# Kernel optimization log

Hardware: AMD Instinct MI355X
Metric: run time of the kernel (lower is better)

The kernel has to match this reference:

```python
import jax, jax.numpy as jnp
import numpy as np
import math

D_K = 64
DROP_P = 0.5

def setup_inputs() -> dict:
    key = jax.random.key(0)
    kq, kk, kv, km = jax.random.split(key, 4)
    B, S, d = 32, 2048, D_K
    Q = jax.random.normal(kq, (B, S, d), dtype=jnp.float32)
    K = jax.random.normal(kk, (B, S, d), dtype=jnp.float32)
    V = jax.random.normal(kv, (B, S, d), dtype=jnp.float32)
    # Bernoulli(keep_prob) mask for training-mode dropout (p=0.5)
    dropout_mask = jax.random.bernoulli(km, 1.0 - DROP_P, (B, S, S))
    return {"Q": Q, "K": K, "V": V, "dropout_mask": dropout_mask}

def reference(Q, K, V, dropout_mask):
    # attn = softmax(Q K^T / sqrt(d_k)); dropout; y = attn V
    scale = 1.0 / math.sqrt(D_K)
    scores = jnp.einsum('bqd,bkd->bqk', Q, K) * scale   # [B,S,S]
    attn = jax.nn.softmax(scores, axis=-1)
    keep_scale = 1.0 / (1.0 - DROP_P)
    attn = jnp.where(dropout_mask, attn * keep_scale, 0.0)
    y = jnp.einsum('bqk,bkd->bqd', attn, V)             # [B,S,d]
    return (y, attn)
```

## Files before the change

kernel.cpp:

```cpp
#include <hip/hip_runtime.h>
#include <hip/hip_bf16.h>
#include <stdint.h>

#define SQ 2048
#define DK 64
#define NB 32
#define TQ 16
#define EW 2064
#define NTHREADS 512
#define SCL 0.18033688011112042f

typedef __attribute__((ext_vector_type(8))) short short8;
typedef __attribute__((ext_vector_type(4))) float f32x4;

__device__ __forceinline__ unsigned f2bf_u(float x) {
    unsigned u = __builtin_bit_cast(unsigned, x);
    u += 0x7fffu + ((u >> 16) & 1u);
    return u >> 16;
}
__device__ __forceinline__ float bf2f(unsigned h) {
    return __builtin_bit_cast(float, h << 16);
}
__device__ __forceinline__ void split8(const float* p, short8& h, short8& l) {
    f32x4 a = *(const f32x4*)p;
    f32x4 b = *(const f32x4*)(p + 4);
    #pragma unroll
    for (int j = 0; j < 4; ++j) {
        unsigned ua = f2bf_u(a[j]);
        h[j] = (short)ua; l[j] = (short)f2bf_u(a[j] - bf2f(ua));
        unsigned ub = f2bf_u(b[j]);
        h[j + 4] = (short)ub; l[j + 4] = (short)f2bf_u(b[j] - bf2f(ub));
    }
}
__device__ __forceinline__ unsigned pkf16(float a, float b) {
    unsigned short ha = __builtin_bit_cast(unsigned short, (_Float16)a);
    unsigned short hb = __builtin_bit_cast(unsigned short, (_Float16)b);
    return (unsigned)ha | ((unsigned)hb << 16);
}
__device__ __forceinline__ float upk16(unsigned u, int hi) {
    return (float)__builtin_bit_cast(_Float16, (unsigned short)(hi ? (u >> 16) : (u & 0xffffu)));
}

__global__ __launch_bounds__(256) void prep_kernel(
    const float* __restrict__ K, const float* __restrict__ V,
    unsigned short* __restrict__ Khi, unsigned short* __restrict__ Klo,
    unsigned short* __restrict__ Vt)
{
    __shared__ float vtile[64][65];
    const int t  = threadIdx.x;
    const int b  = blockIdx.x >> 5;
    const int s0 = (blockIdx.x & 31) << 6;
    const size_t base = ((size_t)b * SQ + s0) * DK + (size_t)t * 16;

    {
        short8 h0, l0, h1, l1;
        split8(K + base,     h0, l0);
        split8(K + base + 8, h1, l1);
        *(short8*)(Khi + base)     = h0;
        *(short8*)(Khi + base + 8) = h1;
        *(short8*)(Klo + base)     = l0;
        *(short8*)(Klo + base + 8) = l1;
    }
    {
        const int sr = t >> 2, dc = (t & 3) << 4;
        #pragma unroll
        for (int u = 0; u < 16; u += 4) {
            f32x4 v = *(const f32x4*)(V + base + u);
            vtile[sr][dc + u + 0] = v[0];
            vtile[sr][dc + u + 1] = v[1];
            vtile[sr][dc + u + 2] = v[2];
            vtile[sr][dc + u + 3] = v[3];
        }
    }
    __syncthreads();
    #pragma unroll
    for (int rep = 0; rep < 16; ++rep) {
        const int idx = rep * 256 + t;
        const int d = idx >> 6, s = idx & 63;
        Vt[((size_t)b * DK + d) * SQ + s0 + s] = (unsigned short)f2bf_u(vtile[s][d]);
    }
}

__global__ __launch_bounds__(NTHREADS, 4) void sdpa_main(
    const float* __restrict__ Q, const unsigned short* __restrict__ Khi,
    const unsigned short* __restrict__ Klo, const unsigned short* __restrict__ Vt,
    const unsigned* __restrict__ Mk, float* __restrict__ Yout, float* __restrict__ Aout)
{
    __shared__ __align__(16) unsigned short e_lds[TQ][EW];
    __shared__ float yp[2][TQ][DK];
    __shared__ float rsum[8][TQ];
    __shared__ float i2s[TQ];

    const int tid  = threadIdx.x;
    const int lane = tid & 63;
    const int wv   = tid >> 6;
    const int m16  = lane & 15;
    const int kq   = lane >> 4;
    const int koff = kq * 8;

    const int b  = blockIdx.x >> 7;
    const int q0 = (blockIdx.x & 127) * TQ;

    short8 qh[2], ql[2];
    {
        const float* qrow = Q + ((size_t)b * SQ + q0 + m16) * DK;
        split8(qrow + koff,      qh[0], ql[0]);
        split8(qrow + 32 + koff, qh[1], ql[1]);
    }

    float rs = 0.f;
    {
        const size_t krow = ((size_t)b * SQ + wv * 256 + m16) * DK;
        const unsigned short* khp = Khi + krow;
        const unsigned short* klp = Klo + krow;
        for (int t = 0; t < 16; ++t) {
            const int off = t * 16 * DK;
            f32x4 acc = {0.f, 0.f, 0.f, 0.f};
            #pragma unroll
            for (int c = 0; c < 2; ++c) {
                short8 kh = *(const short8*)(khp + off + c * 32 + koff);
                short8 kl = *(const short8*)(klp + off + c * 32 + koff);
                acc = __builtin_amdgcn_mfma_f32_16x16x32_bf16(kh, qh[c], acc, 0, 0, 0);
                acc = __builtin_amdgcn_mfma_f32_16x16x32_bf16(kh, ql[c], acc, 0, 0, 0);
                acc = __builtin_amdgcn_mfma_f32_16x16x32_bf16(kl, qh[c], acc, 0, 0, 0);
            }
            const float e0 = exp2f(acc[0] * SCL);
            const float e1 = exp2f(acc[1] * SCL);
            const float e2 = exp2f(acc[2] * SCL);
            const float e3 = exp2f(acc[3] * SCL);
            rs += (e0 + e1) + (e2 + e3);
            uint2 pk;
            pk.x = pkf16(e0, e1);
            pk.y = pkf16(e2, e3);
            *(uint2*)&e_lds[m16][wv * 256 + t * 16 + kq * 4] = pk;
        }
    }
    rs += __shfl_xor(rs, 16);
    rs += __shfl_xor(rs, 32);
    if (lane < 16) rsum[wv][lane] = rs;
    __syncthreads();

    if (tid < 16) {
        float s = 0.f;
        #pragma unroll
        for (int w = 0; w < 8; ++w) s += rsum[w][tid];
        i2s[tid] = 2.0f / s;
    }
    __syncthreads();

    {
        const size_t g0 = ((size_t)b * SQ + q0) * SQ + (size_t)tid * 4;
        #pragma unroll 2
        for (int r = 0; r < TQ; ++r) {
            const uint4 mk = *(const uint4*)(Mk + g0 + (size_t)r * SQ);
            const uint2 ev = *(const uint2*)&e_lds[r][tid * 4];
            const float i2 = i2s[r];
            const float a0 = mk.x ? upk16(ev.x, 0) * i2 : 0.f;
            const float a1 = mk.y ? upk16(ev.x, 1) * i2 : 0.f;
            const float a2 = mk.z ? upk16(ev.y, 0) * i2 : 0.f;
            const float a3 = mk.w ? upk16(ev.y, 1) * i2 : 0.f;
            f32x4 av = {a0, a1, a2, a3};
            *(f32x4*)(Aout + g0 + (size_t)r * SQ) = av;
            uint2 pb;
            pb.x = f2bf_u(a0) | (f2bf_u(a1) << 16);
            pb.y = f2bf_u(a2) | (f2bf_u(a3) << 16);
            *(uint2*)&e_lds[r][tid * 4] = pb;
        }
    }
    __syncthreads();

    {
        const int khalf = wv & 1;
        const int d0 = (wv >> 1) * 16;
        const unsigned short* vrow = Vt + ((size_t)b * DK + d0 + m16) * SQ;
        f32x4 acc = {0.f, 0.f, 0.f, 0.f};
        for (int ch = 0; ch < 32; ++ch) {
            const int k0 = khalf * 1024 + ch * 32;
            short8 af = *(const short8*)&e_lds[m16][k0 + koff];
            short8 vf = *(const short8*)(vrow + k0 + koff);
            acc = __builtin_amdgcn_mfma_f32_16x16x32_bf16(af, vf, acc, 0, 0, 0);
        }
        #pragma unroll
        for (int r = 0; r < 4; ++r)
            yp[khalf][kq * 4 + r][d0 + m16] = acc[r];
    }
    __syncthreads();

    {
        const int q  = tid >> 5;
        const int dd = (tid & 31) * 2;
        float2 yv;
        yv.x = yp[0][q][dd]     + yp[1][q][dd];
        yv.y = yp[0][q][dd + 1] + yp[1][q][dd + 1];
        *(float2*)(Yout + ((size_t)b * SQ + q0 + q) * DK + dd) = yv;
    }
}

extern "C" void kernel_launch(void* const* d_in, const int* in_sizes, int n_in,
                              void* d_out, int out_size, void* d_ws, size_t ws_size,
                              hipStream_t stream) {
    const float*    Q  = (const float*)d_in[0];
    const float*    K  = (const float*)d_in[1];
    const float*    V  = (const float*)d_in[2];
    const unsigned* Mk = (const unsigned*)d_in[3];
    float* Yout = (float*)d_out;
    float* Aout = (float*)d_out + (size_t)NB * SQ * DK;

    const size_t NEL = (size_t)NB * SQ * DK;
    unsigned short* Khi = (unsigned short*)d_ws;
    unsigned short* Klo = Khi + NEL;
    unsigned short* Vt  = Klo + NEL;

    prep_kernel<<<dim3(NB * (SQ / 64)), dim3(256), 0, stream>>>(K, V, Khi, Klo, Vt);
    sdpa_main<<<dim3(NB * (SQ / TQ)), dim3(NTHREADS), 0, stream>>>(
        Q, Khi, Klo, Vt, Mk, Yout, Aout);
}
```

Before: 507.6 us.

## Pipeline mask/attn-finish with PV MFMA per chunk, swizzle LDS, nontemporal IO

The dropout/normalize pass that writes the attention matrix is split into eight 256-column chunks, and each chunk is software-pipelined with the PV MFMA accumulation of the previous chunk. This lets mask loads and attention stores overlap tensor work instead of running as a separate phase. LDS addresses are XOR-swizzled to cut bank conflicts, and mask loads and output stores use nontemporal hints. The Y reduction is also restructured so each wave pair sums its partials. The cost is more barriers (one per chunk) and changed per-thread work mapping.

```diff
diff --git a/kernel.cpp b/kernel.cpp
--- a/kernel.cpp
+++ b/kernel.cpp
@@ -12,6 +12,8 @@
 
 typedef __attribute__((ext_vector_type(8))) short short8;
 typedef __attribute__((ext_vector_type(4))) float f32x4;
+typedef __attribute__((ext_vector_type(4))) unsigned u32x4;
+typedef __attribute__((ext_vector_type(2))) unsigned u32x2;
 
 __device__ __forceinline__ unsigned f2bf_u(float x) {
     unsigned u = __builtin_bit_cast(unsigned, x);
@@ -87,7 +89,7 @@
     const unsigned* __restrict__ Mk, float* __restrict__ Yout, float* __restrict__ Aout)
 {
     __shared__ __align__(16) unsigned short e_lds[TQ][EW];
-    __shared__ float yp[2][TQ][DK];
+    __shared__ float yp[4][TQ][16];
     __shared__ float rsum[8][TQ];
     __shared__ float i2s[TQ];
 
@@ -113,6 +115,7 @@
         const size_t krow = ((size_t)b * SQ + wv * 256 + m16) * DK;
         const unsigned short* khp = Khi + krow;
         const unsigned short* klp = Klo + krow;
+        const int xw = (m16 & 7) << 3;
         for (int t = 0; t < 16; ++t) {
             const int off = t * 16 * DK;
             f32x4 acc = {0.f, 0.f, 0.f, 0.f};
@@ -129,17 +132,16 @@
             const float e2 = exp2f(acc[2] * SCL);
             const float e3 = exp2f(acc[3] * SCL);
             rs += (e0 + e1) + (e2 + e3);
-            uint2 pk;
-            pk.x = pkf16(e0, e1);
-            pk.y = pkf16(e2, e3);
-            *(uint2*)&e_lds[m16][wv * 256 + t * 16 + kq * 4] = pk;
+            u32x2 pk;
+            pk[0] = pkf16(e0, e1);
+            pk[1] = pkf16(e2, e3);
+            *(u32x2*)&e_lds[m16][(wv * 256 + t * 16 + kq * 4) ^ xw] = pk;
         }
     }
     rs += __shfl_xor(rs, 16);
     rs += __shfl_xor(rs, 32);
     if (lane < 16) rsum[wv][lane] = rs;
     __syncthreads();
-
     if (tid < 16) {
         float s = 0.f;
         #pragma unroll
@@ -148,52 +150,80 @@
     }
     __syncthreads();
 
-    {
-        const size_t g0 = ((size_t)b * SQ + q0) * SQ + (size_t)tid * 4;
-        #pragma unroll 2
-        for (int r = 0; r < TQ; ++r) {
-            const uint4 mk = *(const uint4*)(Mk + g0 + (size_t)r * SQ);
-            const uint2 ev = *(const uint2*)&e_lds[r][tid * 4];
-            const float i2 = i2s[r];
-            const float a0 = mk.x ? upk16(ev.x, 0) * i2 : 0.f;
-            const float a1 = mk.y ? upk16(ev.x, 1) * i2 : 0.f;
-            const float a2 = mk.z ? upk16(ev.y, 0) * i2 : 0.f;
-            const float a3 = mk.w ? upk16(ev.y, 1) * i2 : 0.f;
-            f32x4 av = {a0, a1, a2, a3};
-            *(f32x4*)(Aout + g0 + (size_t)r * SQ) = av;
-            uint2 pb;
-            pb.x = f2bf_u(a0) | (f2bf_u(a1) << 16);
-            pb.y = f2bf_u(a2) | (f2bf_u(a3) << 16);
-            *(uint2*)&e_lds[r][tid * 4] = pb;
-        }
-    }
-    __syncthreads();
-
-    {
-        const int khalf = wv & 1;
-        const int d0 = (wv >> 1) * 16;
-        const unsigned short* vrow = Vt + ((size_t)b * DK + d0 + m16) * SQ;
-        f32x4 acc = {0.f, 0.f, 0.f, 0.f};
-        for (int ch = 0; ch < 32; ++ch) {
-            const int k0 = khalf * 1024 + ch * 32;
-            short8 af = *(const short8*)&e_lds[m16][k0 + koff];
+    const int cr = tid >> 5;
+    const int cc = (tid & 31) * 8;
+    const int xc = (cr & 7) << 3;
+    const float i2 = i2s[cr];
+    const size_t crow = ((size_t)b * SQ + q0 + cr) * SQ + cc;
+
+    const int g   = wv >> 1;
+    const int par = wv & 1;
+    const int xm  = (m16 & 7) << 3;
+    const unsigned short* vrow = Vt + ((size_t)b * DK + g * 16 + m16) * SQ;
+    f32x4 acc = {0.f, 0.f, 0.f, 0.f};
+
+    #define C_FINISH(s, ma, mb)                                                   \
+    {                                                                             \
+        unsigned short* ep = &e_lds[cr][((s) * 256 + cc) ^ xc];                   \
+        const u32x4 ev = *(const u32x4*)ep;                                       \
+        const float a0 = (ma)[0] ? upk16(ev[0], 0) * i2 : 0.f;                    \
+        const float a1 = (ma)[1] ? upk16(ev[0], 1) * i2 : 0.f;                    \
+        const float a2 = (ma)[2] ? upk16(ev[1], 0) * i2 : 0.f;                    \
+        const float a3 = (ma)[3] ? upk16(ev[1], 1) * i2 : 0.f;                    \
+        const float a4 = (mb)[0] ? upk16(ev[2], 0) * i2 : 0.f;                    \
+        const float a5 = (mb)[1] ? upk16(ev[2], 1) * i2 : 0.f;                    \
+        const float a6 = (mb)[2] ? upk16(ev[3], 0) * i2 : 0.f;                    \
+        const float a7 = (mb)[3] ? upk16(ev[3], 1) * i2 : 0.f;                    \
+        f32x4 av0 = {a0, a1, a2, a3};                                             \
+        f32x4 av1 = {a4, a5, a6, a7};                                             \
+        __builtin_nontemporal_store(av0, (f32x4*)(Aout + crow + (s) * 256));      \
+        __builtin_nontemporal_store(av1, (f32x4*)(Aout + crow + (s) * 256 + 4));  \
+        u32x4 pb;                                                                 \
+        pb[0] = f2bf_u(a0) | (f2bf_u(a1) << 16);                                  \
+        pb[1] = f2bf_u(a2) | (f2bf_u(a3) << 16);                                  \
+        pb[2] = f2bf_u(a4) | (f2bf_u(a5) << 16);                                  \
+        pb[3] = f2bf_u(a6) | (f2bf_u(a7) << 16);                                  \
+        *(u32x4*)ep = pb;                                                         \
+    }
+
+    {
+        u32x4 ma = __builtin_nontemporal_load((const u32x4*)(Mk + crow));
+        u32x4 mb = __builtin_nontemporal_load((const u32x4*)(Mk + crow + 4));
+        C_FINISH(0, ma, mb);
+    }
+    __syncthreads();
+
+    for (int s = 0; s < 8; ++s) {
+        u32x4 na, nb;
+        if (s < 7) {
+            na = __builtin_nontemporal_load((const u32x4*)(Mk + crow + (s + 1) * 256));
+            nb = __builtin_nontemporal_load((const u32x4*)(Mk + crow + (s + 1) * 256 + 4));
+        }
+        #pragma unroll
+        for (int c = 0; c < 4; ++c) {
+            const int k0 = s * 256 + par * 128 + c * 32;
+            short8 af = *(const short8*)&e_lds[m16][(k0 + koff) ^ xm];
             short8 vf = *(const short8*)(vrow + k0 + koff);
             acc = __builtin_amdgcn_mfma_f32_16x16x32_bf16(af, vf, acc, 0, 0, 0);
         }
-        #pragma unroll
-        for (int r = 0; r < 4; ++r)
-            yp[khalf][kq * 4 + r][d0 + m16] = acc[r];
-    }
-    __syncthreads();
-
-    {
-        const int q  = tid >> 5;
-        const int dd = (tid & 31) * 2;
-        float2 yv;
-        yv.x = yp[0][q][dd]     + yp[1][q][dd];
-        yv.y = yp[0][q][dd + 1] + yp[1][q][dd + 1];
-        *(float2*)(Yout + ((size_t)b * SQ + q0 + q) * DK + dd) = yv;
-    }
+        if (s < 7) C_FINISH(s + 1, na, nb);
+        __syncthreads();
+    }
+
+    if (par == 1) {
+        #pragma unroll
+        for (int r = 0; r < 4; ++r) yp[g][kq * 4 + r][m16] = acc[r];
+    }
+    __syncthreads();
+    if (par == 0) {
+        #pragma unroll
+        for (int r = 0; r < 4; ++r) {
+            const float yv = acc[r] + yp[g][kq * 4 + r][m16];
+            __builtin_nontemporal_store(yv,
+                Yout + ((size_t)b * SQ + q0 + kq * 4 + r) * DK + g * 16 + m16);
+        }
+    }
+    #undef C_FINISH
 }
 
 extern "C" void kernel_launch(void* const* d_in, const int* in_sizes, int n_in,
```

Result: no change. 498.6 us (-1.8%).

## Split fused attention into QK/softmax kernel and separate PV kernel rereading attn

Applied to the files above, without the earlier changes.

Splits the fused kernel in two. The first kernel computes the scores, writes exp values as bf16 into LDS with an XOR swizzle, and emits the dropout-masked attention matrix using nontemporal loads and stores. The second kernel rereads the fp32 attention matrix from global memory, converts it to bf16 and does the PV MFMA to produce Y. Both kernels remap block indices so that each XCD handles whole batches, and the QK MFMA chain is split into two accumulators. The aim is to cut LDS pressure and dependency stalls, at the cost of reading the 512MB attention matrix back from global memory a second time.

```diff
diff --git a/kernel.cpp b/kernel.cpp
--- a/kernel.cpp
+++ b/kernel.cpp
@@ -7,11 +7,12 @@
 #define NB 32
 #define TQ 16
 #define EW 2064
-#define NTHREADS 512
 #define SCL 0.18033688011112042f
 
 typedef __attribute__((ext_vector_type(8))) short short8;
 typedef __attribute__((ext_vector_type(4))) float f32x4;
+typedef __attribute__((ext_vector_type(4))) unsigned u32x4;
+typedef __attribute__((ext_vector_type(2))) unsigned u32x2;
 
 __device__ __forceinline__ unsigned f2bf_u(float x) {
     unsigned u = __builtin_bit_cast(unsigned, x);
@@ -20,6 +21,9 @@
 }
 __device__ __forceinline__ float bf2f(unsigned h) {
     return __builtin_bit_cast(float, h << 16);
+}
+__device__ __forceinline__ float bf2f_hi(unsigned u) {
+    return __builtin_bit_cast(float, u & 0xffff0000u);
 }
 __device__ __forceinline__ void split8(const float* p, short8& h, short8& l) {
     f32x4 a = *(const f32x4*)p;
@@ -31,14 +35,6 @@
         unsigned ub = f2bf_u(b[j]);
         h[j + 4] = (short)ub; l[j + 4] = (short)f2bf_u(b[j] - bf2f(ub));
     }
-}
-__device__ __forceinline__ unsigned pkf16(float a, float b) {
-    unsigned short ha = __builtin_bit_cast(unsigned short, (_Float16)a);
-    unsigned short hb = __builtin_bit_cast(unsigned short, (_Float16)b);
-    return (unsigned)ha | ((unsigned)hb << 16);
-}
-__device__ __forceinline__ float upk16(unsigned u, int hi) {
-    return (float)__builtin_bit_cast(_Float16, (unsigned short)(hi ? (u >> 16) : (u & 0xffffu)));
 }
 
 __global__ __launch_bounds__(256) void prep_kernel(
@@ -81,13 +77,12 @@
     }
 }
 
-__global__ __launch_bounds__(NTHREADS, 4) void sdpa_main(
+__global__ __launch_bounds__(512, 4) void qk_kernel(
     const float* __restrict__ Q, const unsigned short* __restrict__ Khi,
-    const unsigned short* __restrict__ Klo, const unsigned short* __restrict__ Vt,
-    const unsigned* __restrict__ Mk, float* __restrict__ Yout, float* __restrict__ Aout)
+    const unsigned short* __restrict__ Klo, const unsigned* __restrict__ Mk,
+    float* __restrict__ Aout)
 {
     __shared__ __align__(16) unsigned short e_lds[TQ][EW];
-    __shared__ float yp[2][TQ][DK];
     __shared__ float rsum[8][TQ];
     __shared__ float i2s[TQ];
 
@@ -98,8 +93,11 @@
     const int kq   = lane >> 4;
     const int koff = kq * 8;
 
-    const int b  = blockIdx.x >> 7;
-    const int q0 = (blockIdx.x & 127) * TQ;
+    const int bx  = blockIdx.x;
+    const int xcd = bx & 7;
+    const int j   = bx >> 3;
+    const int b   = xcd * 4 + (j >> 7);
+    const int q0  = (j & 127) * TQ;
 
     short8 qh[2], ql[2];
     {
@@ -113,33 +111,36 @@
         const size_t krow = ((size_t)b * SQ + wv * 256 + m16) * DK;
         const unsigned short* khp = Khi + krow;
         const unsigned short* klp = Klo + krow;
+        const int xw = (m16 & 7) << 3;
         for (int t = 0; t < 16; ++t) {
             const int off = t * 16 * DK;
-            f32x4 acc = {0.f, 0.f, 0.f, 0.f};
-            #pragma unroll
-            for (int c = 0; c < 2; ++c) {
-                short8 kh = *(const short8*)(khp + off + c * 32 + koff);
-                short8 kl = *(const short8*)(klp + off + c * 32 + koff);
-                acc = __builtin_amdgcn_mfma_f32_16x16x32_bf16(kh, qh[c], acc, 0, 0, 0);
-                acc = __builtin_amdgcn_mfma_f32_16x16x32_bf16(kh, ql[c], acc, 0, 0, 0);
-                acc = __builtin_amdgcn_mfma_f32_16x16x32_bf16(kl, qh[c], acc, 0, 0, 0);
-            }
-            const float e0 = exp2f(acc[0] * SCL);
-            const float e1 = exp2f(acc[1] * SCL);
-            const float e2 = exp2f(acc[2] * SCL);
-            const float e3 = exp2f(acc[3] * SCL);
+            short8 kh0 = *(const short8*)(khp + off + koff);
+            short8 kh1 = *(const short8*)(khp + off + 32 + koff);
+            short8 kl0 = *(const short8*)(klp + off + koff);
+            short8 kl1 = *(const short8*)(klp + off + 32 + koff);
+            f32x4 a0 = {0.f, 0.f, 0.f, 0.f};
+            f32x4 a1 = {0.f, 0.f, 0.f, 0.f};
+            a0 = __builtin_amdgcn_mfma_f32_16x16x32_bf16(kh0, qh[0], a0, 0, 0, 0);
+            a1 = __builtin_amdgcn_mfma_f32_16x16x32_bf16(kh1, qh[1], a1, 0, 0, 0);
+            a0 = __builtin_amdgcn_mfma_f32_16x16x32_bf16(kh0, ql[0], a0, 0, 0, 0);
+            a1 = __builtin_amdgcn_mfma_f32_16x16x32_bf16(kh1, ql[1], a1, 0, 0, 0);
+            a0 = __builtin_amdgcn_mfma_f32_16x16x32_bf16(kl0, qh[0], a0, 0, 0, 0);
+            a1 = __builtin_amdgcn_mfma_f32_16x16x32_bf16(kl1, qh[1], a1, 0, 0, 0);
+            const float e0 = __builtin_amdgcn_exp2f((a0[0] + a1[0]) * SCL);
+            const float e1 = __builtin_amdgcn_exp2f((a0[1] + a1[1]) * SCL);
+            const float e2 = __builtin_amdgcn_exp2f((a0[2] + a1[2]) * SCL);
+            const float e3 = __builtin_amdgcn_exp2f((a0[3] + a1[3]) * SCL);
             rs += (e0 + e1) + (e2 + e3);
-            uint2 pk;
-            pk.x = pkf16(e0, e1);
-            pk.y = pkf16(e2, e3);
-            *(uint2*)&e_lds[m16][wv * 256 + t * 16 + kq * 4] = pk;
+            u32x2 pk;
+            pk[0] = f2bf_u(e0) | (f2bf_u(e1) << 16);
+            pk[1] = f2bf_u(e2) | (f2bf_u(e3) << 16);
+            *(u32x2*)&e_lds[m16][(wv * 256 + t * 16 + kq * 4) ^ xw] = pk;
         }
     }
     rs += __shfl_xor(rs, 16);
     rs += __shfl_xor(rs, 32);
     if (lane < 16) rsum[wv][lane] = rs;
     __syncthreads();
-
     if (tid < 16) {
         float s = 0.f;
         #pragma unroll
@@ -149,50 +150,85 @@
     __syncthreads();
 
     {
-        const size_t g0 = ((size_t)b * SQ + q0) * SQ + (size_t)tid * 4;
-        #pragma unroll 2
-        for (int r = 0; r < TQ; ++r) {
-            const uint4 mk = *(const uint4*)(Mk + g0 + (size_t)r * SQ);
-            const uint2 ev = *(const uint2*)&e_lds[r][tid * 4];
-            const float i2 = i2s[r];
-            const float a0 = mk.x ? upk16(ev.x, 0) * i2 : 0.f;
-            const float a1 = mk.y ? upk16(ev.x, 1) * i2 : 0.f;
-            const float a2 = mk.z ? upk16(ev.y, 0) * i2 : 0.f;
-            const float a3 = mk.w ? upk16(ev.y, 1) * i2 : 0.f;
-            f32x4 av = {a0, a1, a2, a3};
-            *(f32x4*)(Aout + g0 + (size_t)r * SQ) = av;
-            uint2 pb;
-            pb.x = f2bf_u(a0) | (f2bf_u(a1) << 16);
-            pb.y = f2bf_u(a2) | (f2bf_u(a3) << 16);
-            *(uint2*)&e_lds[r][tid * 4] = pb;
-        }
-    }
-    __syncthreads();
-
-    {
-        const int khalf = wv & 1;
-        const int d0 = (wv >> 1) * 16;
-        const unsigned short* vrow = Vt + ((size_t)b * DK + d0 + m16) * SQ;
-        f32x4 acc = {0.f, 0.f, 0.f, 0.f};
-        for (int ch = 0; ch < 32; ++ch) {
-            const int k0 = khalf * 1024 + ch * 32;
-            short8 af = *(const short8*)&e_lds[m16][k0 + koff];
+        const int cr = tid >> 5;
+        const int cc = (tid & 31) * 8;
+        const int xc = (cr & 7) << 3;
+        const float i2 = i2s[cr];
+        const size_t crow = ((size_t)b * SQ + q0 + cr) * SQ + cc;
+        #pragma unroll
+        for (int s = 0; s < 8; ++s) {
+            const u32x4 ma = __builtin_nontemporal_load((const u32x4*)(Mk + crow + s * 256));
+            const u32x4 mb = __builtin_nontemporal_load((const u32x4*)(Mk + crow + s * 256 + 4));
+            const u32x4 ev = *(const u32x4*)&e_lds[cr][(s * 256 + cc) ^ xc];
+            f32x4 o0, o1;
+            o0[0] = ma[0] ? bf2f(ev[0] & 0xffffu) * i2 : 0.f;
+            o0[1] = ma[1] ? bf2f_hi(ev[0]) * i2 : 0.f;
+            o0[2] = ma[2] ? bf2f(ev[1] & 0xffffu) * i2 : 0.f;
+            o0[3] = ma[3] ? bf2f_hi(ev[1]) * i2 : 0.f;
+            o1[0] = mb[0] ? bf2f(ev[2] & 0xffffu) * i2 : 0.f;
+            o1[1] = mb[1] ? bf2f_hi(ev[2]) * i2 : 0.f;
+            o1[2] = mb[2] ? bf2f(ev[3] & 0xffffu) * i2 : 0.f;
+            o1[3] = mb[3] ? bf2f_hi(ev[3]) * i2 : 0.f;
+            __builtin_nontemporal_store(o0, (f32x4*)(Aout + crow + s * 256));
+            __builtin_nontemporal_store(o1, (f32x4*)(Aout + crow + s * 256 + 4));
+        }
+    }
+}
+
+__global__ __launch_bounds__(256, 8) void pv_kernel(
+    const float* __restrict__ Attn, const unsigned short* __restrict__ Vt,
+    float* __restrict__ Yout)
+{
+    const int tid  = threadIdx.x;
+    const int lane = tid & 63;
+    const int g    = tid >> 6;
+    const int m16  = lane & 15;
+    const int kq   = lane >> 4;
+    const int koff = kq * 8;
+
+    const int bx  = blockIdx.x;
+    const int xcd = bx & 7;
+    const int j   = bx >> 3;
+    const int b   = xcd * 4 + (j >> 7);
+    const int q0  = (j & 127) * TQ;
+
+    const float*          arow = Attn + ((size_t)b * SQ + q0 + m16) * SQ;
+    const unsigned short* vrow = Vt + ((size_t)b * DK + g * 16 + m16) * SQ;
+
+    f32x4 accA = {0.f, 0.f, 0.f, 0.f};
+    f32x4 accB = {0.f, 0.f, 0.f, 0.f};
+    #pragma unroll 8
+    for (int ch = 0; ch < 64; ch += 2) {
+        {
+            const int k0 = ch * 32;
+            f32x4 p0 = *(const f32x4*)(arow + k0 + koff);
+            f32x4 p1 = *(const f32x4*)(arow + k0 + koff + 4);
+            short8 af;
+            af[0] = (short)f2bf_u(p0[0]); af[1] = (short)f2bf_u(p0[1]);
+            af[2] = (short)f2bf_u(p0[2]); af[3] = (short)f2bf_u(p0[3]);
+            af[4] = (short)f2bf_u(p1[0]); af[5] = (short)f2bf_u(p1[1]);
+            af[6] = (short)f2bf_u(p1[2]); af[7] = (short)f2bf_u(p1[3]);
             short8 vf = *(const short8*)(vrow + k0 + koff);
-            acc = __builtin_amdgcn_mfma_f32_16x16x32_bf16(af, vf, acc, 0, 0, 0);
-        }
-        #pragma unroll
-        for (int r = 0; r < 4; ++r)
-            yp[khalf][kq * 4 + r][d0 + m16] = acc[r];
-    }
-    __syncthreads();
-
-    {
-        const int q  = tid >> 5;
-        const int dd = (tid & 31) * 2;
-        float2 yv;
-        yv.x = yp[0][q][dd]     + yp[1][q][dd];
-        yv.y = yp[0][q][dd + 1] + yp[1][q][dd + 1];
-        *(float2*)(Yout + ((size_t)b * SQ + q0 + q) * DK + dd) = yv;
+            accA = __builtin_amdgcn_mfma_f32_16x16x32_bf16(af, vf, accA, 0, 0, 0);
+        }
+        {
+            const int k0 = (ch + 1) * 32;
+            f32x4 p0 = *(const f32x4*)(arow + k0 + koff);
+            f32x4 p1 = *(const f32x4*)(arow + k0 + koff + 4);
+            short8 af;
+            af[0] = (short)f2bf_u(p0[0]); af[1] = (short)f2bf_u(p0[1]);
+            af[2] = (short)f2bf_u(p0[2]); af[3] = (short)f2bf_u(p0[3]);
+            af[4] = (short)f2bf_u(p1[0]); af[5] = (short)f2bf_u(p1[1]);
+            af[6] = (short)f2bf_u(p1[2]); af[7] = (short)f2bf_u(p1[3]);
+            short8 vf = *(const short8*)(vrow + k0 + koff);
+            accB = __builtin_amdgcn_mfma_f32_16x16x32_bf16(af, vf, accB, 0, 0, 0);
+        }
+    }
+    #pragma unroll
+    for (int r = 0; r < 4; ++r) {
+        const float yv = accA[r] + accB[r];
+        __builtin_nontemporal_store(yv,
+            Yout + ((size_t)b * SQ + q0 + kq * 4 + r) * DK + g * 16 + m16);
     }
 }
 
@@ -212,6 +248,6 @@
     unsigned short* Vt  = Klo + NEL;
 
     prep_kernel<<<dim3(NB * (SQ / 64)), dim3(256), 0, stream>>>(K, V, Khi, Klo, Vt);
-    sdpa_main<<<dim3(NB * (SQ / TQ)), dim3(NTHREADS), 0, stream>>>(
-        Q, Khi, Klo, Vt, Mk, Yout, Aout);
-}
+    qk_kernel<<<dim3(NB * (SQ / TQ)), dim3(512), 0, stream>>>(Q, Khi, Klo, Mk, Aout);
+    pv_kernel<<<dim3(NB * (SQ / TQ)), dim3(256), 0, stream>>>(Aout, Vt, Yout);
+}
```

Result: slower. 770.1 us (+51.7%).

## Split softmax into two passes with precomputed row sums and bit-packed dropout mask

Applied to the files above, without the earlier changes.

Adds a prep pass that packs the 32-bit dropout mask into bitmasks and computes per-row softmax normalizers with a first QK^T pass. The main kernel then recomputes QK^T per tile and applies normalization, mask and PV in a streaming loop over 32-query tiles. This removes the full-row LDS buffer and the serialized phases within a block. In exchange it reads the full mask in a separate pass, computes QK^T twice, and reduces Y through LDS atomics. Block-to-batch mapping is arranged by XCD and attention output uses nontemporal stores.

```diff
diff --git a/kernel.cpp b/kernel.cpp
--- a/kernel.cpp
+++ b/kernel.cpp
@@ -5,13 +5,12 @@
 #define SQ 2048
 #define DK 64
 #define NB 32
-#define TQ 16
-#define EW 2064
-#define NTHREADS 512
 #define SCL 0.18033688011112042f
 
 typedef __attribute__((ext_vector_type(8))) short short8;
 typedef __attribute__((ext_vector_type(4))) float f32x4;
+typedef __attribute__((ext_vector_type(4))) unsigned u32x4;
+typedef __attribute__((ext_vector_type(2))) unsigned u32x2;
 
 __device__ __forceinline__ unsigned f2bf_u(float x) {
     unsigned u = __builtin_bit_cast(unsigned, x);
@@ -20,6 +19,11 @@
 }
 __device__ __forceinline__ float bf2f(unsigned h) {
     return __builtin_bit_cast(float, h << 16);
+}
+__device__ __forceinline__ unsigned cvtpk_bf16(float lo, float hi) {
+    unsigned r;
+    asm("v_cvt_pk_bf16_f32 %0, %1, %2" : "=v"(r) : "v"(lo), "v"(hi));
+    return r;
 }
 __device__ __forceinline__ void split8(const float* p, short8& h, short8& l) {
     f32x4 a = *(const f32x4*)p;
@@ -31,14 +35,6 @@
         unsigned ub = f2bf_u(b[j]);
         h[j + 4] = (short)ub; l[j + 4] = (short)f2bf_u(b[j] - bf2f(ub));
     }
-}
-__device__ __forceinline__ unsigned pkf16(float a, float b) {
-    unsigned short ha = __builtin_bit_cast(unsigned short, (_Float16)a);
-    unsigned short hb = __builtin_bit_cast(unsigned short, (_Float16)b);
-    return (unsigned)ha | ((unsigned)hb << 16);
-}
-__device__ __forceinline__ float upk16(unsigned u, int hi) {
-    return (float)__builtin_bit_cast(_Float16, (unsigned short)(hi ? (u >> 16) : (u & 0xffffu)));
 }
 
 __global__ __launch_bounds__(256) void prep_kernel(
@@ -81,15 +77,107 @@
     }
 }
 
-__global__ __launch_bounds__(NTHREADS, 4) void sdpa_main(
+__global__ __launch_bounds__(256) void prep2_kernel(
+    const float* __restrict__ Q, const unsigned short* __restrict__ Khi,
+    const unsigned short* __restrict__ Klo, const unsigned* __restrict__ Mk,
+    unsigned* __restrict__ Mkb, float* __restrict__ I2)
+{
+    __shared__ float rsum2[4][32];
+    const int t = threadIdx.x;
+
+    if (blockIdx.x < 16384) {
+        const size_t w = (size_t)blockIdx.x * 256 + t;
+        const unsigned* p = Mk + w * 32;
+        unsigned bits = 0;
+        #pragma unroll
+        for (int jj = 0; jj < 8; ++jj) {
+            const u32x4 v = *(const u32x4*)(p + jj * 4);
+            bits |= (v[0] ? 1u : 0u) << (jj * 4 + 0);
+            bits |= (v[1] ? 1u : 0u) << (jj * 4 + 1);
+            bits |= (v[2] ? 1u : 0u) << (jj * 4 + 2);
+            bits |= (v[3] ? 1u : 0u) << (jj * 4 + 3);
+        }
+        Mkb[w] = bits;
+        return;
+    }
+
+    const int bid2 = blockIdx.x - 16384;
+    const int xcd = bid2 & 7;
+    const int j   = bid2 >> 3;
+    const int b   = xcd * 4 + (j >> 6);
+    const int q0  = (j & 63) * 32;
+
+    const int lane = t & 63;
+    const int wv   = t >> 6;
+    const int m16  = lane & 15;
+    const int koff = (lane >> 4) * 8;
+
+    short8 qh0[2], ql0[2], qh1[2], ql1[2];
+    {
+        const float* qr0 = Q + ((size_t)b * SQ + q0 + m16) * DK;
+        split8(qr0 + koff,      qh0[0], ql0[0]);
+        split8(qr0 + 32 + koff, qh0[1], ql0[1]);
+        const float* qr1 = qr0 + 16 * DK;
+        split8(qr1 + koff,      qh1[0], ql1[0]);
+        split8(qr1 + 32 + koff, qh1[1], ql1[1]);
+    }
+    const size_t krow = ((size_t)b * SQ + wv * 512 + m16) * DK;
+    const unsigned short* khp = Khi + krow;
+    const unsigned short* klp = Klo + krow;
+
+    float rs0 = 0.f, rs1 = 0.f;
+    #pragma unroll 8
+    for (int tt = 0; tt < 32; ++tt) {
+        const int off = tt * 16 * DK;
+        const short8 kh0 = *(const short8*)(khp + off + koff);
+        const short8 kh1 = *(const short8*)(khp + off + 32 + koff);
+        const short8 kl0 = *(const short8*)(klp + off + koff);
+        const short8 kl1 = *(const short8*)(klp + off + 32 + koff);
+        {
+            f32x4 c0 = {0.f,0.f,0.f,0.f}, c1 = {0.f,0.f,0.f,0.f};
+            c0 = __builtin_amdgcn_mfma_f32_16x16x32_bf16(kh0, qh0[0], c0, 0, 0, 0);
+            c1 = __builtin_amdgcn_mfma_f32_16x16x32_bf16(kh1, qh0[1], c1, 0, 0, 0);
+            c0 = __builtin_amdgcn_mfma_f32_16x16x32_bf16(kh0, ql0[0], c0, 0, 0, 0);
+            c1 = __builtin_amdgcn_mfma_f32_16x16x32_bf16(kh1, ql0[1], c1, 0, 0, 0);
+            c0 = __builtin_amdgcn_mfma_f32_16x16x32_bf16(kl0, qh0[0], c0, 0, 0, 0);
+            c1 = __builtin_amdgcn_mfma_f32_16x16x32_bf16(kl1, qh0[1], c1, 0, 0, 0);
+            rs0 += (__builtin_amdgcn_exp2f((c0[0]+c1[0])*SCL) + __builtin_amdgcn_exp2f((c0[1]+c1[1])*SCL))
+                 + (__builtin_amdgcn_exp2f((c0[2]+c1[2])*SCL) + __builtin_amdgcn_exp2f((c0[3]+c1[3])*SCL));
+        }
+        {
+            f32x4 c0 = {0.f,0.f,0.f,0.f}, c1 = {0.f,0.f,0.f,0.f};
+            c0 = __builtin_amdgcn_mfma_f32_16x16x32_bf16(kh0, qh1[0], c0, 0, 0, 0);
+            c1 = __builtin_amdgcn_mfma_f32_16x16x32_bf16(kh1, qh1[1], c1, 0, 0, 0);
+            c0 = __builtin_amdgcn_mfma_f32_16x16x32_bf16(kh0, ql1[0], c0, 0, 0, 0);
+            c1 = __builtin_amdgcn_mfma_f32_16x16x32_bf16(kh1, ql1[1], c1, 0, 0, 0);
+            c0 = __builtin_amdgcn_mfma_f32_16x16x32_bf16(kl0, qh1[0], c0, 0, 0, 0);
+            c1 = __builtin_amdgcn_mfma_f32_16x16x32_bf16(kl1, qh1[1], c1, 0, 0, 0);
+            rs1 += (__builtin_amdgcn_exp2f((c0[0]+c1[0])*SCL) + __builtin_amdgcn_exp2f((c0[1]+c1[1])*SCL))
+                 + (__builtin_amdgcn_exp2f((c0[2]+c1[2])*SCL) + __builtin_amdgcn_exp2f((c0[3]+c1[3])*SCL));
+        }
+    }
+    rs0 += __shfl_xor(rs0, 16);  rs0 += __shfl_xor(rs0, 32);
+    rs1 += __shfl_xor(rs1, 16);  rs1 += __shfl_xor(rs1, 32);
+    if (lane < 16) {
+        rsum2[wv][lane]      = rs0;
+        rsum2[wv][16 + lane] = rs1;
+    }
+    __syncthreads();
+    if (t < 32) {
+        const float s = (rsum2[0][t] + rsum2[1][t]) + (rsum2[2][t] + rsum2[3][t]);
+        I2[(size_t)b * SQ + q0 + t] = 2.0f / s;
+    }
+}
+
+__global__ __launch_bounds__(512, 4) void sdpa_main(
     const float* __restrict__ Q, const unsigned short* __restrict__ Khi,
     const unsigned short* __restrict__ Klo, const unsigned short* __restrict__ Vt,
-    const unsigned* __restrict__ Mk, float* __restrict__ Yout, float* __restrict__ Aout)
+    const unsigned* __restrict__ Mkb, const float* __restrict__ I2,
+    float* __restrict__ Yout, float* __restrict__ Aout)
 {
-    __shared__ __align__(16) unsigned short e_lds[TQ][EW];
-    __shared__ float yp[2][TQ][DK];
-    __shared__ float rsum[8][TQ];
-    __shared__ float i2s[TQ];
+    __shared__ __align__(16) float astage[8][2][16][36];
+    __shared__ __align__(16) unsigned short pstage[8][2][16][36];
+    __shared__ float yp[32][68];
 
     const int tid  = threadIdx.x;
     const int lane = tid & 63;
@@ -98,101 +186,134 @@
     const int kq   = lane >> 4;
     const int koff = kq * 8;
 
-    const int b  = blockIdx.x >> 7;
-    const int q0 = (blockIdx.x & 127) * TQ;
-
-    short8 qh[2], ql[2];
-    {
-        const float* qrow = Q + ((size_t)b * SQ + q0 + m16) * DK;
-        split8(qrow + koff,      qh[0], ql[0]);
-        split8(qrow + 32 + koff, qh[1], ql[1]);
-    }
-
-    float rs = 0.f;
-    {
-        const size_t krow = ((size_t)b * SQ + wv * 256 + m16) * DK;
-        const unsigned short* khp = Khi + krow;
-        const unsigned short* klp = Klo + krow;
-        for (int t = 0; t < 16; ++t) {
-            const int off = t * 16 * DK;
-            f32x4 acc = {0.f, 0.f, 0.f, 0.f};
-            #pragma unroll
-            for (int c = 0; c < 2; ++c) {
-                short8 kh = *(const short8*)(khp + off + c * 32 + koff);
-                short8 kl = *(const short8*)(klp + off + c * 32 + koff);
-                acc = __builtin_amdgcn_mfma_f32_16x16x32_bf16(kh, qh[c], acc, 0, 0, 0);
-                acc = __builtin_amdgcn_mfma_f32_16x16x32_bf16(kh, ql[c], acc, 0, 0, 0);
-                acc = __builtin_amdgcn_mfma_f32_16x16x32_bf16(kl, qh[c], acc, 0, 0, 0);
-            }
-            const float e0 = exp2f(acc[0] * SCL);
-            const float e1 = exp2f(acc[1] * SCL);
-            const float e2 = exp2f(acc[2] * SCL);
-            const float e3 = exp2f(acc[3] * SCL);
-            rs += (e0 + e1) + (e2 + e3);
-            uint2 pk;
-            pk.x = pkf16(e0, e1);
-            pk.y = pkf16(e2, e3);
-            *(uint2*)&e_lds[m16][wv * 256 + t * 16 + kq * 4] = pk;
-        }
-    }
-    rs += __shfl_xor(rs, 16);
-    rs += __shfl_xor(rs, 32);
-    if (lane < 16) rsum[wv][lane] = rs;
+    const int bx  = blockIdx.x;
+    const int xcd = bx & 7;
+    const int j   = bx >> 3;
+    const int b   = xcd * 4 + (j >> 6);
+    const int q0  = (j & 63) * 32;
+
+    for (int i = tid; i < 32 * 68; i += 512) ((float*)yp)[i] = 0.f;
+
+    short8 qh0[2], ql0[2], qh1[2], ql1[2];
+    {
+        const float* qr0 = Q + ((size_t)b * SQ + q0 + m16) * DK;
+        split8(qr0 + koff,      qh0[0], ql0[0]);
+        split8(qr0 + 32 + koff, qh0[1], ql0[1]);
+        const float* qr1 = qr0 + 16 * DK;
+        split8(qr1 + koff,      qh1[0], ql1[0]);
+        split8(qr1 + 32 + koff, qh1[1], ql1[1]);
+    }
+    const float i2r0 = I2[(size_t)b * SQ + q0 + m16];
+    const float i2r1 = I2[(size_t)b * SQ + q0 + 16 + m16];
+
+    const unsigned* mrow0 = Mkb + ((size_t)b * SQ + q0 + m16) * (SQ / 32) + wv * 8;
+    const unsigned* mrow1 = mrow0 + (size_t)16 * (SQ / 32);
+
+    const size_t krow = ((size_t)b * SQ + wv * 256 + m16) * DK;
+    const unsigned short* khp = Khi + krow;
+    const unsigned short* klp = Klo + krow;
+
+    f32x4 A00={0.f,0.f,0.f,0.f}, A01={0.f,0.f,0.f,0.f}, A02={0.f,0.f,0.f,0.f}, A03={0.f,0.f,0.f,0.f};
+    f32x4 A10={0.f,0.f,0.f,0.f}, A11={0.f,0.f,0.f,0.f}, A12={0.f,0.f,0.f,0.f}, A13={0.f,0.f,0.f,0.f};
+
     __syncthreads();
 
-    if (tid < 16) {
-        float s = 0.f;
-        #pragma unroll
-        for (int w = 0; w < 8; ++w) s += rsum[w][tid];
-        i2s[tid] = 2.0f / s;
-    }
+    #define QKSTEP(h, s2, K0, K1, L0, L1, QH, QL, I2R, MW)                        \
+    {                                                                             \
+        f32x4 c0 = {0.f,0.f,0.f,0.f}, c1 = {0.f,0.f,0.f,0.f};                     \
+        c0 = __builtin_amdgcn_mfma_f32_16x16x32_bf16(K0, QH[0], c0, 0, 0, 0);     \
+        c1 = __builtin_amdgcn_mfma_f32_16x16x32_bf16(K1, QH[1], c1, 0, 0, 0);     \
+        c0 = __builtin_amdgcn_mfma_f32_16x16x32_bf16(K0, QL[0], c0, 0, 0, 0);     \
+        c1 = __builtin_amdgcn_mfma_f32_16x16x32_bf16(K1, QL[1], c1, 0, 0, 0);     \
+        c0 = __builtin_amdgcn_mfma_f32_16x16x32_bf16(L0, QH[0], c0, 0, 0, 0);     \
+        c1 = __builtin_amdgcn_mfma_f32_16x16x32_bf16(L1, QH[1], c1, 0, 0, 0);     \
+        const float e0 = __builtin_amdgcn_exp2f((c0[0] + c1[0]) * SCL);           \
+        const float e1 = __builtin_amdgcn_exp2f((c0[1] + c1[1]) * SCL);           \
+        const float e2 = __builtin_amdgcn_exp2f((c0[2] + c1[2]) * SCL);           \
+        const float e3 = __builtin_amdgcn_exp2f((c0[3] + c1[3]) * SCL);           \
+        const unsigned bits = ((MW) >> ((s2) * 16 + kq * 4)) & 0xfu;              \
+        const float p0 = (bits & 1u) ? e0 * (I2R) : 0.f;                          \
+        const float p1 = (bits & 2u) ? e1 * (I2R) : 0.f;                          \
+        const float p2 = (bits & 4u) ? e2 * (I2R) : 0.f;                          \
+        const float p3 = (bits & 8u) ? e3 * (I2R) : 0.f;                          \
+        f32x4 pv = {p0, p1, p2, p3};                                              \
+        *(f32x4*)&astage[wv][h][m16][(s2) * 16 + kq * 4] = pv;                    \
+        u32x2 pk;                                                                 \
+        pk[0] = cvtpk_bf16(p0, p1);                                               \
+        pk[1] = cvtpk_bf16(p2, p3);                                               \
+        *(u32x2*)&pstage[wv][h][m16][(s2) * 16 + kq * 4] = pk;                    \
+    }
+
+    #define PVH(h, AA0, AA1, AA2, AA3, kbase)                                     \
+    {                                                                             \
+        const short8 af = *(const short8*)&pstage[wv][h][m16][koff];              \
+        const unsigned short* vb = Vt + ((size_t)b * DK + m16) * SQ + (kbase) + koff; \
+        AA0 = __builtin_amdgcn_mfma_f32_16x16x32_bf16(af, *(const short8*)vb, AA0, 0, 0, 0); \
+        AA1 = __builtin_amdgcn_mfma_f32_16x16x32_bf16(af, *(const short8*)(vb + (size_t)16 * SQ), AA1, 0, 0, 0); \
+        AA2 = __builtin_amdgcn_mfma_f32_16x16x32_bf16(af, *(const short8*)(vb + (size_t)32 * SQ), AA2, 0, 0, 0); \
+        AA3 = __builtin_amdgcn_mfma_f32_16x16x32_bf16(af, *(const short8*)(vb + (size_t)48 * SQ), AA3, 0, 0, 0); \
+    }
+
+    #define STH(h, kbase)                                                         \
+    {                                                                             \
+        const int r  = lane >> 2;                                                 \
+        const int c8 = (lane & 3) * 8;                                            \
+        const f32x4 o0 = *(const f32x4*)&astage[wv][h][r][c8];                    \
+        const f32x4 o1 = *(const f32x4*)&astage[wv][h][r][c8 + 4];                \
+        float* ap = Aout + ((size_t)b * SQ + q0 + (h) * 16 + r) * SQ + (kbase) + c8; \
+        __builtin_nontemporal_store(o0, (f32x4*)ap);                              \
+        __builtin_nontemporal_store(o1, (f32x4*)(ap + 4));                        \
+    }
+
+    #define PP_ITER(pp)                                                           \
+    {                                                                             \
+        const int kbase = wv * 256 + (pp) * 32;                                   \
+        const int offa = ((pp) * 2) * 16 * DK, offb = ((pp) * 2 + 1) * 16 * DK;   \
+        const short8 ka0 = *(const short8*)(khp + offa + koff);                   \
+        const short8 ka1 = *(const short8*)(khp + offa + 32 + koff);              \
+        const short8 la0 = *(const short8*)(klp + offa + koff);                   \
+        const short8 la1 = *(const short8*)(klp + offa + 32 + koff);              \
+        const short8 kb0 = *(const short8*)(khp + offb + koff);                   \
+        const short8 kb1 = *(const short8*)(khp + offb + 32 + koff);              \
+        const short8 lb0 = *(const short8*)(klp + offb + koff);                   \
+        const short8 lb1 = *(const short8*)(klp + offb + 32 + koff);              \
+        const unsigned mw0 = mrow0[(pp)];                                         \
+        const unsigned mw1 = mrow1[(pp)];                                         \
+        QKSTEP(0, 0, ka0, ka1, la0, la1, qh0, ql0, i2r0, mw0)                     \
+        QKSTEP(0, 1, kb0, kb1, lb0, lb1, qh0, ql0, i2r0, mw0)                     \
+        QKSTEP(1, 0, ka0, ka1, la0, la1, qh1, ql1, i2r1, mw1)                     \
+        QKSTEP(1, 1, kb0, kb1, lb0, lb1, qh1, ql1, i2r1, mw1)                     \
+        PVH(0, A00, A01, A02, A03, kbase)                                         \
+        PVH(1, A10, A11, A12, A13, kbase)                                         \
+        STH(0, kbase)                                                             \
+        STH(1, kbase)                                                             \
+    }
+
+    PP_ITER(0) PP_ITER(1) PP_ITER(2) PP_ITER(3)
+    PP_ITER(4) PP_ITER(5) PP_ITER(6) PP_ITER(7)
+
+    #undef PP_ITER
+    #undef STH
+    #undef PVH
+    #undef QKSTEP
+
+    #define YACC(h, g, AC)                                                        \
+    {                                                                             \
+        _Pragma("unroll")                                                         \
+        for (int r = 0; r < 4; ++r)                                               \
+            atomicAdd(&yp[(h) * 16 + kq * 4 + r][(g) * 16 + m16], AC[r]);         \
+    }
+    YACC(0, 0, A00) YACC(0, 1, A01) YACC(0, 2, A02) YACC(0, 3, A03)
+    YACC(1, 0, A10) YACC(1, 1, A11) YACC(1, 2, A12) YACC(1, 3, A13)
+    #undef YACC
     __syncthreads();
 
     {
-        const size_t g0 = ((size_t)b * SQ + q0) * SQ + (size_t)tid * 4;
-        #pragma unroll 2
-        for (int r = 0; r < TQ; ++r) {
-            const uint4 mk = *(const uint4*)(Mk + g0 + (size_t)r * SQ);
-            const uint2 ev = *(const uint2*)&e_lds[r][tid * 4];
-            const float i2 = i2s[r];
-            const float a0 = mk.x ? upk16(ev.x, 0) * i2 : 0.f;
-            const float a1 = mk.y ? upk16(ev.x, 1) * i2 : 0.f;
-            const float a2 = mk.z ? upk16(ev.y, 0) * i2 : 0.f;
-            const float a3 = mk.w ? upk16(ev.y, 1) * i2 : 0.f;
-            f32x4 av = {a0, a1, a2, a3};
-            *(f32x4*)(Aout + g0 + (size_t)r * SQ) = av;
-            uint2 pb;
-            pb.x = f2bf_u(a0) | (f2bf_u(a1) << 16);
-            pb.y = f2bf_u(a2) | (f2bf_u(a3) << 16);
-            *(uint2*)&e_lds[r][tid * 4] = pb;
-        }
-    }
-    __syncthreads();
-
-    {
-        const int khalf = wv & 1;
-        const int d0 = (wv >> 1) * 16;
-        const unsigned short* vrow = Vt + ((size_t)b * DK + d0 + m16) * SQ;
-        f32x4 acc = {0.f, 0.f, 0.f, 0.f};
-        for (int ch = 0; ch < 32; ++ch) {
-            const int k0 = khalf * 1024 + ch * 32;
-            short8 af = *(const short8*)&e_lds[m16][k0 + koff];
-            short8 vf = *(const short8*)(vrow + k0 + koff);
-            acc = __builtin_amdgcn_mfma_f32_16x16x32_bf16(af, vf, acc, 0, 0, 0);
-        }
-        #pragma unroll
-        for (int r = 0; r < 4; ++r)
-            yp[khalf][kq * 4 + r][d0 + m16] = acc[r];
-    }
-    __syncthreads();
-
-    {
-        const int q  = tid >> 5;
-        const int dd = (tid & 31) * 2;
-        float2 yv;
-        yv.x = yp[0][q][dd]     + yp[1][q][dd];
-        yv.y = yp[0][q][dd + 1] + yp[1][q][dd + 1];
-        *(float2*)(Yout + ((size_t)b * SQ + q0 + q) * DK + dd) = yv;
+        const int q  = tid >> 4;
+        const int d4 = (tid & 15) * 4;
+        const f32x4 yv = *(const f32x4*)&yp[q][d4];
+        __builtin_nontemporal_store(yv,
+            (f32x4*)(Yout + ((size_t)b * SQ + q0 + q) * DK + d4));
     }
 }
 
@@ -210,8 +331,11 @@
     unsigned short* Khi = (unsigned short*)d_ws;
     unsigned short* Klo = Khi + NEL;
     unsigned short* Vt  = Klo + NEL;
-
-    prep_kernel<<<dim3(NB * (SQ / 64)), dim3(256), 0, stream>>>(K, V, Khi, Klo, Vt);
-    sdpa_main<<<dim3(NB * (SQ / TQ)), dim3(NTHREADS), 0, stream>>>(
-        Q, Khi, Klo, Vt, Mk, Yout, Aout);
-}
+    unsigned*       Mkb = (unsigned*)(Vt + NEL);
+    float*          I2  = (float*)(Mkb + (size_t)NB * SQ * (SQ / 32));
+
+    prep_kernel<<<dim3(NB * 32), dim3(256), 0, stream>>>(K, V, Khi, Klo, Vt);
+    prep2_kernel<<<dim3(16384 + 2048), dim3(256), 0, stream>>>(Q, Khi, Klo, Mk, Mkb, I2);
+    sdpa_main<<<dim3(NB * (SQ / 32)), dim3(512), 0, stream>>>(
+        Q, Khi, Klo, Vt, Mkb, I2, Yout, Aout);
+}
```

Result: slower. 739.3 us (+45.7%).
